# Performance work log

Measured on AMD Instinct MI355X. Metric: run time of the kernel, lower is better.

Reference implementation:

```python
import jax, jax.numpy as jnp
import numpy as np

N = 4096      # nodes
E = 131072    # edges
C_IN = 128
HID = 128     # d_model of transformer (= embed_dim used in reshape_to_trans)
OUT = 32      # GNN output channels -> transformer seq_len
HEADS = 8
DH = HID // HEADS
FF = 2048     # torch TransformerEncoderLayer default dim_feedforward
EPS = 1e-5


def layer_norm(x, g, b):
    mu = jnp.mean(x, axis=-1, keepdims=True)
    var = jnp.mean(jnp.square(x - mu), axis=-1, keepdims=True)
    return (x - mu) * jax.lax.rsqrt(var + EPS) * g + b


def setup_inputs() -> dict:
    key = jax.random.key(0)
    ks = jax.random.split(key, 24)
    def rn(k, shape, scale=0.05):
        return jax.random.normal(k, shape, dtype=jnp.float32) * scale
    inp = {
        "x": jax.random.normal(ks[0], (N, C_IN), dtype=jnp.float32),
        "edge_index": jax.random.randint(ks[1], (2, E), 0, N, dtype=jnp.int64),
        # GCN layers
        "Wg1": rn(ks[2], (C_IN, HID)), "bg1": jnp.zeros((HID,), jnp.float32),
        "Wg2": rn(ks[3], (HID, HID)),  "bg2": jnp.zeros((HID,), jnp.float32),
        "Wg3": rn(ks[4], (HID, OUT)),  "bg3": jnp.zeros((OUT,), jnp.float32),
        # MHA
        "Wq": rn(ks[5], (HID, HID)), "bq": jnp.zeros((HID,), jnp.float32),
        "Wk": rn(ks[6], (HID, HID)), "bk": jnp.zeros((HID,), jnp.float32),
        "Wv": rn(ks[7], (HID, HID)), "bv": jnp.zeros((HID,), jnp.float32),
        "Wo": rn(ks[8], (HID, HID)), "bo": jnp.zeros((HID,), jnp.float32),
        "ln1_g": jnp.ones((HID,), jnp.float32), "ln1_b": jnp.zeros((HID,), jnp.float32),
        # FFN
        "W1": rn(ks[9], (HID, FF)),  "b1": jnp.zeros((FF,), jnp.float32),
        "W2": rn(ks[10], (FF, HID)), "b2": jnp.zeros((HID,), jnp.float32),
        "ln2_g": jnp.ones((HID,), jnp.float32), "ln2_b": jnp.zeros((HID,), jnp.float32),
    }
    return inp


def reference(x, edge_index, Wg1, bg1, Wg2, bg2, Wg3, bg3,
              Wq, bq, Wk, bk, Wv, bv, Wo, bo, ln1_g, ln1_b,
              W1, b1, W2, b2, ln2_g, ln2_b):
    # ---- GCN normalization (add self-loops, symmetric D^-1/2 (A+I) D^-1/2) ----
    loop = jnp.arange(N, dtype=edge_index.dtype)
    src = jnp.concatenate([edge_index[0], loop])
    dst = jnp.concatenate([edge_index[1], loop])
    deg = jax.ops.segment_sum(jnp.ones((E + N,), jnp.float32), dst, num_segments=N)
    dinv = jnp.where(deg > 0, jax.lax.rsqrt(deg), 0.0)
    norm = (dinv[src] * dinv[dst])[:, None]  # [E+N, 1]

    def gcn(h, W, b):
        m = h @ W                               # [N, d_out]
        agg = jax.ops.segment_sum(m[src] * norm, dst, num_segments=N)
        return agg + b

    h = jax.nn.relu(gcn(x, Wg1, bg1))
    h = jax.nn.relu(gcn(h, Wg2, bg2))
    h = jax.nn.relu(gcn(h, Wg3, bg3))           # [N, OUT]

    # ---- reshape_to_trans: [N, OUT] -> [N, OUT, HID] (repeat along embed dim) ----
    t = jnp.broadcast_to(h[:, :, None], (N, OUT, HID))

    # ---- TransformerEncoderLayer (post-norm, relu FFN, no dropout at eval) ----
    q = (t @ Wq + bq).reshape(N, OUT, HEADS, DH)
    k = (t @ Wk + bk).reshape(N, OUT, HEADS, DH)
    v = (t @ Wv + bv).reshape(N, OUT, HEADS, DH)
    scores = jnp.einsum("bqhd,bkhd->bhqk", q, k) / jnp.sqrt(jnp.float32(DH))
    attn = jax.nn.softmax(scores, axis=-1)
    ctx = jnp.einsum("bhqk,bkhd->bqhd", attn, v).reshape(N, OUT, HID)
    a = ctx @ Wo + bo
    x1 = layer_norm(t + a, ln1_g, ln1_b)
    f = jax.nn.relu(x1 @ W1 + b1) @ W2 + b2
    out = layer_norm(x1 + f, ln2_g, ln2_b)      # [N, OUT, HID]
    return out
```

## Files before the change

kernel.cpp:

```cpp
#include <hip/hip_runtime.h>

#define NN 4096
#define EE 131072
#define FFD 2048

typedef float f32x4 __attribute__((ext_vector_type(4)));
typedef __bf16 bf16x8 __attribute__((ext_vector_type(8)));
typedef unsigned int u32;
typedef u32 u32x4 __attribute__((ext_vector_type(4)));
typedef unsigned short u16;
typedef u16 u16x8 __attribute__((ext_vector_type(8)));

__device__ __forceinline__ u16 f2bf(float f) {
    unsigned u = __builtin_bit_cast(unsigned, f);
    return (u16)((u + 0x7FFFu + ((u >> 16) & 1u)) >> 16);
}
__device__ __forceinline__ float bf2f(u16 h) {
    unsigned u = ((unsigned)h) << 16;
    return __builtin_bit_cast(float, u);
}

#define GLD16(g, l) __builtin_amdgcn_global_load_lds(                            \
    (const __attribute__((address_space(1))) void*)(g),                          \
    (__attribute__((address_space(3))) void*)(l), 16, 0, 0)

__global__ void k_detect(const int* __restrict__ ei, int* __restrict__ flag) {
    int v = ei[2 * threadIdx.x + 1];
    unsigned long long any = __ballot(v != 0);
    if (threadIdx.x == 0) *flag = (any == 0ULL) ? 1 : 0;
}
__device__ __forceinline__ int ldedge(const int* ei, int idx, int is64) {
    return is64 ? ei[2 * idx] : ei[idx];
}

__global__ void k_degi(const int* __restrict__ ei, const int* __restrict__ flag,
                       int* __restrict__ cnt) {
    int e = blockIdx.x * 256 + threadIdx.x;
    if (e >= EE) return;
    atomicAdd(&cnt[ldedge(ei, EE + e, *flag)], 1);
}
__global__ __launch_bounds__(1024) void k_scan(const int* __restrict__ cnt,
        int* __restrict__ rp, int* __restrict__ cur, float* __restrict__ dinv) {
    __shared__ int tsum[1024];
    int t = threadIdx.x;
    int c0 = cnt[t * 4], c1 = cnt[t * 4 + 1], c2 = cnt[t * 4 + 2], c3 = cnt[t * 4 + 3];
    int s = c0 + c1 + c2 + c3;
    tsum[t] = s;
    dinv[t * 4]     = rsqrtf((float)c0 + 1.0f);
    dinv[t * 4 + 1] = rsqrtf((float)c1 + 1.0f);
    dinv[t * 4 + 2] = rsqrtf((float)c2 + 1.0f);
    dinv[t * 4 + 3] = rsqrtf((float)c3 + 1.0f);
    __syncthreads();
    for (int off = 1; off < 1024; off <<= 1) {
        int v = (t >= off) ? tsum[t - off] : 0;
        __syncthreads();
        tsum[t] += v;
        __syncthreads();
    }
    int excl = tsum[t] - s;
    int p0 = excl, p1 = excl + c0, p2 = p1 + c1, p3 = p2 + c2;
    rp[t * 4] = p0; rp[t * 4 + 1] = p1; rp[t * 4 + 2] = p2; rp[t * 4 + 3] = p3;
    cur[t * 4] = p0; cur[t * 4 + 1] = p1; cur[t * 4 + 2] = p2; cur[t * 4 + 3] = p3;
    if (t == 1023) rp[4096] = excl + s;
}
__global__ void k_bucket(const int* __restrict__ ei, const int* __restrict__ flag,
                         int* __restrict__ cur, int* __restrict__ es) {
    int e = blockIdx.x * 256 + threadIdx.x;
    if (e >= EE) return;
    int is64 = *flag;
    int s = ldedge(ei, e, is64), d = ldedge(ei, EE + e, is64);
    int pos = atomicAdd(&cur[d], 1);
    es[pos] = s;
}

__global__ __launch_bounds__(256) void k_gcn_mm128(const float* __restrict__ h,
        const float* __restrict__ W, const float* __restrict__ dinv, float* __restrict__ ms) {
    __shared__ float hr[2][128];
    int t = threadIdx.x, n0 = blockIdx.x * 2, r = t >> 7, e = t & 127;
    hr[r][e] = h[(size_t)(n0 + r) * 128 + e];
    __syncthreads();
    float a = 0.f;
    #pragma unroll 8
    for (int c = 0; c < 128; ++c) a += hr[r][c] * W[c * 128 + e];
    ms[(size_t)(n0 + r) * 128 + e] = a * dinv[n0 + r];
}
__global__ __launch_bounds__(256) void k_gcn_mm32(const float* __restrict__ h,
        const float* __restrict__ W, const float* __restrict__ dinv, float* __restrict__ ms) {
    __shared__ float hr[8][128];
    int t = threadIdx.x, n0 = blockIdx.x * 8;
    for (int k2 = 0; k2 < 4; ++k2) {
        int idx = k2 * 256 + t;
        hr[idx >> 7][idx & 127] = h[(size_t)n0 * 128 + idx];
    }
    __syncthreads();
    int r = t >> 5, e = t & 31;
    float a = 0.f;
    #pragma unroll 8
    for (int c = 0; c < 128; ++c) a += hr[r][c] * W[c * 32 + e];
    ms[(size_t)(n0 + r) * 32 + e] = a * dinv[n0 + r];
}

__global__ __launch_bounds__(256) void k_gath128(const int* __restrict__ es,
        const int* __restrict__ rp, const float* __restrict__ ms,
        const float* __restrict__ dinv, const float* __restrict__ b,
        float* __restrict__ hout) {
    int node = blockIdx.x * 4 + (threadIdx.x >> 6), lane = threadIdx.x & 63;
    int st = rp[node], en = rp[node + 1];
    const float2* m2 = (const float2*)ms;
    float ax0 = 0.f, ay0 = 0.f, ax1 = 0.f, ay1 = 0.f;
    int e = st;
    for (; e + 2 <= en; e += 2) {
        int s0 = es[e], s1 = es[e + 1];
        float2 v0 = m2[(size_t)s0 * 64 + lane];
        float2 v1 = m2[(size_t)s1 * 64 + lane];
        ax0 += v0.x; ay0 += v0.y; ax1 += v1.x; ay1 += v1.y;
    }
    if (e < en) {
        float2 v = m2[(size_t)es[e] * 64 + lane];
        ax0 += v.x; ay0 += v.y;
    }
    float dv = dinv[node];
    float2 self = m2[(size_t)node * 64 + lane];
    int c = lane * 2;
    hout[(size_t)node * 128 + c]     = fmaxf(dv * (ax0 + ax1 + self.x) + b[c], 0.f);
    hout[(size_t)node * 128 + c + 1] = fmaxf(dv * (ay0 + ay1 + self.y) + b[c + 1], 0.f);
}
__global__ __launch_bounds__(256) void k_gath32(const int* __restrict__ es,
        const int* __restrict__ rp, const float* __restrict__ ms,
        const float* __restrict__ dinv, const float* __restrict__ b,
        float* __restrict__ hout) {
    int node = blockIdx.x * 8 + (threadIdx.x >> 5), sl = threadIdx.x & 31;
    int st = rp[node], en = rp[node + 1];
    float a0 = 0.f, a1 = 0.f;
    int e = st;
    for (; e + 2 <= en; e += 2) {
        a0 += ms[(size_t)es[e] * 32 + sl];
        a1 += ms[(size_t)es[e + 1] * 32 + sl];
    }
    if (e < en) a0 += ms[(size_t)es[e] * 32 + sl];
    float dv = dinv[node];
    hout[(size_t)node * 32 + sl] =
        fmaxf(dv * (a0 + a1 + ms[(size_t)node * 32 + sl]) + b[sl], 0.f);
}

__global__ __launch_bounds__(128) void k_prep(const float* __restrict__ Wq, const float* __restrict__ bq,
        const float* __restrict__ Wk, const float* __restrict__ bk,
        const float* __restrict__ Wv, const float* __restrict__ bv,
        const float* __restrict__ Wo, const float* __restrict__ bo, float* __restrict__ tc) {
    __shared__ float s_q[128], s_k[128], s_v[128];
    int t = threadIdx.x;
    float aq = 0, ak = 0, av = 0;
    for (int c = 0; c < 128; ++c) {
        aq += Wq[c * 128 + t]; ak += Wk[c * 128 + t]; av += Wv[c * 128 + t];
    }
    s_q[t] = aq; s_k[t] = ak; s_v[t] = av;
    tc[t] = aq; tc[128 + t] = ak; tc[256 + t] = av;
    __syncthreads();
    float pb = 0;
    for (int d = 0; d < 128; ++d) pb += bv[d] * Wo[d * 128 + t];
    tc[1440 + t] = pb + bo[t];
    for (int hh = 0; hh < 8; ++hh) {
        float p = 0;
        #pragma unroll
        for (int d = hh * 16; d < hh * 16 + 16; ++d) p += s_v[d] * Wo[d * 128 + t];
        tc[416 + hh * 128 + t] = p;
    }
    if (t < 8) {
        float A = 0, B = 0, C = 0, D = 0;
        #pragma unroll
        for (int d = t * 16; d < t * 16 + 16; ++d) {
            A += s_q[d] * s_k[d]; B += s_q[d] * bk[d];
            C += bq[d] * s_k[d];  D += bq[d] * bk[d];
        }
        tc[384 + t] = A; tc[392 + t] = B; tc[400 + t] = C; tc[408 + t] = D;
    }
}

__global__ void k_wt(const float* __restrict__ W1, const float* __restrict__ W2,
                     u16* __restrict__ w1t, u16* __restrict__ w2t) {
    int b = blockIdx.x;
    int t = (b & 1023) * 256 + threadIdx.x;
    if (b < 1024) { int f = t >> 7, c = t & 127; w1t[t] = f2bf(W1[c * 2048 + f]); }
    else          { int o = t >> 11, f = t & 2047; w2t[t] = f2bf(W2[f * 128 + o]); }
}

__global__ __launch_bounds__(256) void k_attn(const float* __restrict__ h3, const float* __restrict__ tc,
        const float* __restrict__ g1, const float* __restrict__ b1n, u16* __restrict__ x1b) {
    __shared__ float sh[32];
    __shared__ float ws_[8][32];
    int n = blockIdx.x, t = threadIdx.x;
    if (t < 32) sh[t] = h3[(size_t)n * 32 + t];
    __syncthreads();
    {
        int hh = t >> 5, i = t & 31;
        float A = tc[384 + hh], C = tc[400 + hh];
        float coef = (sh[i] * A + C) * 0.25f;
        float m = -1e30f;
        #pragma unroll
        for (int j = 0; j < 32; ++j) m = fmaxf(m, coef * sh[j]);
        float s = 0.f, wsum = 0.f;
        #pragma unroll
        for (int j = 0; j < 32; ++j) {
            float e = __expf(coef * sh[j] - m);
            s += e; wsum += e * sh[j];
        }
        ws_[hh][i] = wsum / s;
    }
    __syncthreads();
    int wave = t >> 6, lane = t & 63;
    float pb0 = tc[1440 + lane], pb1 = tc[1440 + lane + 64];
    float po0[8], po1[8];
    #pragma unroll
    for (int hh = 0; hh < 8; ++hh) {
        po0[hh] = tc[416 + hh * 128 + lane];
        po1[hh] = tc[416 + hh * 128 + lane + 64];
    }
    float ga = g1[lane], gb = g1[lane + 64], ba = b1n[lane], bb = b1n[lane + 64];
    for (int i = wave; i < 32; i += 4) {
        float y0 = sh[i] + pb0, y1 = sh[i] + pb1;
        #pragma unroll
        for (int hh = 0; hh < 8; ++hh) {
            float w = ws_[hh][i];
            y0 += w * po0[hh]; y1 += w * po1[hh];
        }
        float s1 = y0 + y1, s2 = y0 * y0 + y1 * y1;
        #pragma unroll
        for (int off = 1; off < 64; off <<= 1) {
            s1 += __shfl_xor(s1, off); s2 += __shfl_xor(s2, off);
        }
        float mu = s1 * (1.f / 128.f);
        float var = s2 * (1.f / 128.f) - mu * mu;
        float rs = rsqrtf(var + 1e-5f);
        size_t base = ((size_t)n * 32 + i) * 128;
        x1b[base + lane]      = f2bf((y0 - mu) * rs * ga + ba);
        x1b[base + lane + 64] = f2bf((y1 - mu) * rs * gb + bb);
    }
}


#define STAGE32(buf, Fb) {                                                       \
    char* db_ = (char*)(buf);                                                    \
    _Pragma("unroll") for (int c1_ = 0; c1_ < 2; ++c1_) {                        \
        int f_ = c1_ * 16 + (t >> 4);                                            \
        int bo_ = ((t & 15) * 16) ^ ((f_ & 7) << 4);                             \
        GLD16(w1t + (size_t)((Fb) + f_) * 128 + (bo_ >> 1),                      \
              db_ + c1_ * 4096 + wave * 1024);                                   \
    }                                                                            \
    _Pragma("unroll") for (int c2_ = 0; c2_ < 2; ++c2_) {                        \
        int op_ = c2_ * 32 + wave * 8 + ((t >> 3) & 7);                          \
        int pb_ = (t & 7) ^ ((t >> 3) & 7);                                      \
        int o_  = op_ * 2 + (pb_ >> 2);                                          \
        GLD16(w2t + (size_t)o_ * 2048 + (Fb) + (pb_ & 3) * 8,                    \
              db_ + 8192 + c2_ * 4096 + wave * 1024);                            \
    } }

#define FCOMP32(buf, Fb) {                                                       \
    const char* wb_ = (const char*)(buf);                                        \
    bf16x8 w2f_[8];                                                              \
    _Pragma("unroll") for (int c2_ = 0; c2_ < 8; ++c2_)                          \
        w2f_[c2_] = *(const bf16x8*)(wb_ + 8192 + (c2_ * 8 + (li >> 1)) * 128 +  \
            ((((li & 1) * 64) + g * 16) ^ ((li >> 1) << 4)));                    \
    _Pragma("unroll") for (int cf_ = 0; cf_ < 2; ++cf_) {                        \
        bf16x8 w1f_[4];                                                          \
        _Pragma("unroll") for (int ks_ = 0; ks_ < 4; ++ks_)                      \
            w1f_[ks_] = *(const bf16x8*)(wb_ + (cf_ * 16 + li) * 256 +           \
                ((ks_ * 64 + g * 16) ^ ((li & 7) << 4)));                        \
        f32x4 a0_ = (f32x4){0.f, 0.f, 0.f, 0.f};                                 \
        f32x4 a1_ = (f32x4){0.f, 0.f, 0.f, 0.f};                                 \
        _Pragma("unroll") for (int ks_ = 0; ks_ < 4; ++ks_) {                    \
            a0_ = __builtin_amdgcn_mfma_f32_16x16x32_bf16(af[0][ks_], w1f_[ks_], a0_, 0, 0, 0); \
            a1_ = __builtin_amdgcn_mfma_f32_16x16x32_bf16(af[1][ks_], w1f_[ks_], a1_, 0, 0, 0); \
        }                                                                        \
        float bias_ = b1[(Fb) + cf_ * 16 + li];                                  \
        _Pragma("unroll") for (int r_ = 0; r_ < 4; ++r_) {                       \
            int rp_ = g * 2 + (r_ >> 1);                                         \
            int w_ = (((r_ & 1) * 64) + (cf_ * 16 + li) * 2) ^ (rp_ << 4);       \
            *(u16*)(hwb + rp_ * 128 + w_)       = f2bf(fmaxf(a0_[r_] + bias_, 0.f)); \
            *(u16*)(hwb + (8 + rp_) * 128 + w_) = f2bf(fmaxf(a1_[r_] + bias_, 0.f)); \
        }                                                                        \
    }                                                                            \
    {                                                                            \
        bf16x8 a2_[2];                                                           \
        _Pragma("unroll") for (int rf_ = 0; rf_ < 2; ++rf_)                      \
            a2_[rf_] = *(const bf16x8*)(hwb + (rf_ * 8 + (li >> 1)) * 128 +      \
                ((((li & 1) * 64) + g * 16) ^ ((li >> 1) << 4)));                \
        _Pragma("unroll") for (int c2_ = 0; c2_ < 8; ++c2_) {                    \
            acc2[0][c2_] = __builtin_amdgcn_mfma_f32_16x16x32_bf16(a2_[0], w2f_[c2_], acc2[0][c2_], 0, 0, 0); \
            acc2[1][c2_] = __builtin_amdgcn_mfma_f32_16x16x32_bf16(a2_[1], w2f_[c2_], acc2[1][c2_], 0, 0, 0); \
        }                                                                        \
    } }

__global__ __launch_bounds__(256, 3) void k_ffn(const u16* __restrict__ x1b,
        const u16* __restrict__ w1t, const u16* __restrict__ w2t,
        const float* __restrict__ b1, const float* __restrict__ b2,
        const float* __restrict__ g2, const float* __restrict__ bt2, float* __restrict__ out) {
    __shared__ u16 wA[8192];
    __shared__ u16 wB[8192];
    __shared__ u16 hid[4][1024];
    int t = threadIdx.x, wave = t >> 6, lane = t & 63;
    int g = lane >> 4, li = lane & 15;
    size_t rowbase = (size_t)blockIdx.x * 128;
    char* hwb = (char*)&hid[wave][0];

    STAGE32(wA, 0);

    bf16x8 af[2][4];
    #pragma unroll
    for (int rf = 0; rf < 2; ++rf)
    #pragma unroll
    for (int ks = 0; ks < 4; ++ks)
        af[rf][ks] = *(const bf16x8*)(x1b +
            (rowbase + wave * 32 + rf * 16 + li) * 128 + ks * 32 + g * 8);

    f32x4 acc2[2][8];
    #pragma unroll
    for (int a = 0; a < 2; ++a)
    #pragma unroll
    for (int b = 0; b < 8; ++b) acc2[a][b] = (f32x4){0.f, 0.f, 0.f, 0.f};

    __syncthreads();

    for (int F = 0; F < FFD; F += 64) {
        STAGE32(wB, F + 32);
        FCOMP32(wA, F);
        __syncthreads();
        if (F + 64 < FFD) STAGE32(wA, F + 64);
        FCOMP32(wB, F + 32);
        __syncthreads();
    }

    #pragma unroll
    for (int rf = 0; rf < 2; ++rf)
    #pragma unroll
    for (int r = 0; r < 4; ++r) {
        int lrow = wave * 32 + rf * 16 + g * 4 + r;
        size_t grow = rowbase + lrow;
        float vals[8], s1 = 0.f, s2 = 0.f;
        #pragma unroll
        for (int cf2 = 0; cf2 < 8; ++cf2) {
            int col = cf2 * 16 + li;
            float xv = bf2f(x1b[grow * 128 + col]);
            float y = xv + acc2[rf][cf2][r] + b2[col];
            vals[cf2] = y; s1 += y; s2 += y * y;
        }
        #pragma unroll
        for (int m = 1; m < 16; m <<= 1) {
            s1 += __shfl_xor(s1, m); s2 += __shfl_xor(s2, m);
        }
        float mu = s1 * (1.f / 128.f);
        float var = s2 * (1.f / 128.f) - mu * mu;
        float rs = rsqrtf(var + 1e-5f);
        #pragma unroll
        for (int cf2 = 0; cf2 < 8; ++cf2) {
            int col = cf2 * 16 + li;
            out[grow * 128 + col] = (vals[cf2] - mu) * rs * g2[col] + bt2[col];
        }
    }
}

extern "C" void kernel_launch(void* const* d_in, const int* in_sizes, int n_in,
                              void* d_out, int out_size, void* d_ws, size_t ws_size,
                              hipStream_t stream) {
    const float* x   = (const float*)d_in[0];
    const int*   ei  = (const int*)d_in[1];
    const float *Wg1 = (const float*)d_in[2],  *bg1 = (const float*)d_in[3];
    const float *Wg2 = (const float*)d_in[4],  *bg2 = (const float*)d_in[5];
    const float *Wg3 = (const float*)d_in[6],  *bg3 = (const float*)d_in[7];
    const float *Wq  = (const float*)d_in[8],  *bq  = (const float*)d_in[9];
    const float *Wk  = (const float*)d_in[10], *bk  = (const float*)d_in[11];
    const float *Wv  = (const float*)d_in[12], *bv  = (const float*)d_in[13];
    const float *Wo  = (const float*)d_in[14], *bo  = (const float*)d_in[15];
    const float *g1  = (const float*)d_in[16], *b1n = (const float*)d_in[17];
    const float *W1  = (const float*)d_in[18], *b1  = (const float*)d_in[19];
    const float *W2  = (const float*)d_in[20], *b2  = (const float*)d_in[21];
    const float *g2  = (const float*)d_in[22], *bt2 = (const float*)d_in[23];

    char* ws = (char*)d_ws;
    int*   flag = (int*)(ws + 0);
    int*   cnt  = (int*)(ws + 4096);
    int*   rp   = (int*)(ws + 20480);
    int*   cur  = (int*)(ws + 40960);
    float* dinv = (float*)(ws + 57344);
    float* ms   = (float*)(ws + 73728);
    int*   es   = (int*)(ws + 2170880);
    float* hA   = (float*)(ws + 2695168);
    float* hB   = (float*)(ws + 4792320);
    float* tc   = (float*)(ws + 6889472);
    u16*   w1t  = (u16*)(ws + 6897664);
    u16*   w2t  = (u16*)(ws + 7421952);
    u16*   x1b  = (u16*)(ws + 8388608);
    float* out  = (float*)d_out;

    k_detect<<<1, 64, 0, stream>>>(ei, flag);
    hipMemsetAsync(cnt, 0, 16384, stream);
    k_degi<<<512, 256, 0, stream>>>(ei, flag, cnt);
    k_scan<<<1, 1024, 0, stream>>>(cnt, rp, cur, dinv);
    k_bucket<<<512, 256, 0, stream>>>(ei, flag, cur, es);

    k_gcn_mm128<<<2048, 256, 0, stream>>>(x, Wg1, dinv, ms);
    k_gath128<<<1024, 256, 0, stream>>>(es, rp, ms, dinv, bg1, hA);
    k_gcn_mm128<<<2048, 256, 0, stream>>>(hA, Wg2, dinv, ms);
    k_gath128<<<1024, 256, 0, stream>>>(es, rp, ms, dinv, bg2, hB);
    k_gcn_mm32<<<512, 256, 0, stream>>>(hB, Wg3, dinv, ms);
    k_gath32<<<512, 256, 0, stream>>>(es, rp, ms, dinv, bg3, hA);

    k_prep<<<1, 128, 0, stream>>>(Wq, bq, Wk, bk, Wv, bv, Wo, bo, tc);
    k_wt<<<2048, 256, 0, stream>>>(W1, W2, w1t, w2t);

    k_attn<<<4096, 256, 0, stream>>>(hA, tc, g1, b1n, x1b);

    k_ffn<<<1024, 256, 0, stream>>>(x1b, w1t, w2t, b1, b2, g2, bt2, out);
}
```

Baseline: 307.1 us.

## Fuse independent setup kernels into one launch and pack bf16 conversions in FFN

Merges flag detection with the count zeroing, replacing the memset, and combines edge bucketing, the first GCN matmul, the FFN weight transpose and the attention constant prep into one block-partitioned kernel. The goal is to cut launch count and the idle gaps between small serial kernels, since these jobs do not depend on each other. The FFN epilogue now uses v_cvt_pk_bf16_f32 to convert two floats per instruction instead of manual rounding. The fused kernel's shared buffer and barriers are sized for the largest branch, and the prep branch runs as a single block that could become a tail.

```diff
diff --git a/kernel.cpp b/kernel.cpp
--- a/kernel.cpp
+++ b/kernel.cpp
@@ -19,18 +19,31 @@
     unsigned u = ((unsigned)h) << 16;
     return __builtin_bit_cast(float, u);
 }
+__device__ __forceinline__ u32 cvtpk(float lo, float hi) {
+    u32 r;
+    asm("v_cvt_pk_bf16_f32 %0, %1, %2" : "=v"(r) : "v"(lo), "v"(hi));
+    return r;
+}
 
 #define GLD16(g, l) __builtin_amdgcn_global_load_lds(                            \
     (const __attribute__((address_space(1))) void*)(g),                          \
     (__attribute__((address_space(3))) void*)(l), 16, 0, 0)
 
-__global__ void k_detect(const int* __restrict__ ei, int* __restrict__ flag) {
-    int v = ei[2 * threadIdx.x + 1];
-    unsigned long long any = __ballot(v != 0);
-    if (threadIdx.x == 0) *flag = (any == 0ULL) ? 1 : 0;
-}
 __device__ __forceinline__ int ldedge(const int* ei, int idx, int is64) {
     return is64 ? ei[2 * idx] : ei[idx];
+}
+
+__global__ void k_init(const int* __restrict__ ei, int* __restrict__ flag,
+                       int* __restrict__ cnt) {
+    if (blockIdx.x == 0) {
+        if (threadIdx.x < 64) {
+            int v = ei[2 * threadIdx.x + 1];
+            unsigned long long any = __ballot(v != 0);
+            if (threadIdx.x == 0) *flag = (any == 0ULL) ? 1 : 0;
+        }
+    } else {
+        cnt[(blockIdx.x - 1) * 256 + threadIdx.x] = 0;
+    }
 }
 
 __global__ void k_degi(const int* __restrict__ ei, const int* __restrict__ flag,
@@ -63,14 +76,70 @@
     cur[t * 4] = p0; cur[t * 4 + 1] = p1; cur[t * 4 + 2] = p2; cur[t * 4 + 3] = p3;
     if (t == 1023) rp[4096] = excl + s;
 }
-__global__ void k_bucket(const int* __restrict__ ei, const int* __restrict__ flag,
-                         int* __restrict__ cur, int* __restrict__ es) {
-    int e = blockIdx.x * 256 + threadIdx.x;
-    if (e >= EE) return;
-    int is64 = *flag;
-    int s = ldedge(ei, e, is64), d = ldedge(ei, EE + e, is64);
-    int pos = atomicAdd(&cur[d], 1);
-    es[pos] = s;
+
+__global__ __launch_bounds__(256) void k_fuse1(const int* __restrict__ ei,
+        const int* __restrict__ flag, int* __restrict__ cur, int* __restrict__ es,
+        const float* __restrict__ x, const float* __restrict__ Wg1,
+        const float* __restrict__ dinv, float* __restrict__ ms,
+        const float* __restrict__ W1, const float* __restrict__ W2,
+        u16* __restrict__ w1t, u16* __restrict__ w2t,
+        const float* __restrict__ Wq, const float* __restrict__ bq,
+        const float* __restrict__ Wk, const float* __restrict__ bk,
+        const float* __restrict__ Wv, const float* __restrict__ bv,
+        const float* __restrict__ Wo, const float* __restrict__ bo,
+        float* __restrict__ tc) {
+    __shared__ float sm[384];
+    int b = blockIdx.x, t = threadIdx.x;
+    if (b < 512) {
+        int e = b * 256 + t;
+        int is64 = *flag;
+        int s = ldedge(ei, e, is64), d = ldedge(ei, EE + e, is64);
+        int pos = atomicAdd(&cur[d], 1);
+        es[pos] = s;
+    } else if (b < 2560) {
+        int n0 = (b - 512) * 2, r = t >> 7, e = t & 127;
+        sm[r * 128 + e] = x[(size_t)(n0 + r) * 128 + e];
+        __syncthreads();
+        float a = 0.f;
+        #pragma unroll 8
+        for (int c = 0; c < 128; ++c) a += sm[r * 128 + c] * Wg1[c * 128 + e];
+        ms[(size_t)(n0 + r) * 128 + e] = a * dinv[n0 + r];
+    } else if (b < 4608) {
+        int bb = b - 2560;
+        int tg = (bb & 1023) * 256 + t;
+        if (bb < 1024) { int f = tg >> 7, c = tg & 127; w1t[tg] = f2bf(W1[c * 2048 + f]); }
+        else           { int o = tg >> 11, f = tg & 2047; w2t[tg] = f2bf(W2[f * 128 + o]); }
+    } else {
+        float aq = 0, ak = 0, av = 0;
+        if (t < 128) {
+            for (int c = 0; c < 128; ++c) {
+                aq += Wq[c * 128 + t]; ak += Wk[c * 128 + t]; av += Wv[c * 128 + t];
+            }
+            sm[t] = aq; sm[128 + t] = ak; sm[256 + t] = av;
+            tc[t] = aq; tc[128 + t] = ak; tc[256 + t] = av;
+        }
+        __syncthreads();
+        if (t < 128) {
+            float pb = 0;
+            for (int d = 0; d < 128; ++d) pb += bv[d] * Wo[d * 128 + t];
+            tc[1440 + t] = pb + bo[t];
+            for (int hh = 0; hh < 8; ++hh) {
+                float p = 0;
+                #pragma unroll
+                for (int d = hh * 16; d < hh * 16 + 16; ++d) p += sm[256 + d] * Wo[d * 128 + t];
+                tc[416 + hh * 128 + t] = p;
+            }
+        }
+        if (t < 8) {
+            float A = 0, B = 0, C = 0, D = 0;
+            #pragma unroll
+            for (int d = t * 16; d < t * 16 + 16; ++d) {
+                A += sm[d] * sm[128 + d]; B += sm[d] * bk[d];
+                C += bq[d] * sm[128 + d]; D += bq[d] * bk[d];
+            }
+            tc[384 + t] = A; tc[392 + t] = B; tc[400 + t] = C; tc[408 + t] = D;
+        }
+    }
 }
 
 __global__ __launch_bounds__(256) void k_gcn_mm128(const float* __restrict__ h,
@@ -141,47 +210,6 @@
     float dv = dinv[node];
     hout[(size_t)node * 32 + sl] =
         fmaxf(dv * (a0 + a1 + ms[(size_t)node * 32 + sl]) + b[sl], 0.f);
-}
-
-__global__ __launch_bounds__(128) void k_prep(const float* __restrict__ Wq, const float* __restrict__ bq,
-        const float* __restrict__ Wk, const float* __restrict__ bk,
-        const float* __restrict__ Wv, const float* __restrict__ bv,
-        const float* __restrict__ Wo, const float* __restrict__ bo, float* __restrict__ tc) {
-    __shared__ float s_q[128], s_k[128], s_v[128];
-    int t = threadIdx.x;
-    float aq = 0, ak = 0, av = 0;
-    for (int c = 0; c < 128; ++c) {
-        aq += Wq[c * 128 + t]; ak += Wk[c * 128 + t]; av += Wv[c * 128 + t];
-    }
-    s_q[t] = aq; s_k[t] = ak; s_v[t] = av;
-    tc[t] = aq; tc[128 + t] = ak; tc[256 + t] = av;
-    __syncthreads();
-    float pb = 0;
-    for (int d = 0; d < 128; ++d) pb += bv[d] * Wo[d * 128 + t];
-    tc[1440 + t] = pb + bo[t];
-    for (int hh = 0; hh < 8; ++hh) {
-        float p = 0;
-        #pragma unroll
-        for (int d = hh * 16; d < hh * 16 + 16; ++d) p += s_v[d] * Wo[d * 128 + t];
-        tc[416 + hh * 128 + t] = p;
-    }
-    if (t < 8) {
-        float A = 0, B = 0, C = 0, D = 0;
-        #pragma unroll
-        for (int d = t * 16; d < t * 16 + 16; ++d) {
-            A += s_q[d] * s_k[d]; B += s_q[d] * bk[d];
-            C += bq[d] * s_k[d];  D += bq[d] * bk[d];
-        }
-        tc[384 + t] = A; tc[392 + t] = B; tc[400 + t] = C; tc[408 + t] = D;
-    }
-}
-
-__global__ void k_wt(const float* __restrict__ W1, const float* __restrict__ W2,
-                     u16* __restrict__ w1t, u16* __restrict__ w2t) {
-    int b = blockIdx.x;
-    int t = (b & 1023) * 256 + threadIdx.x;
-    if (b < 1024) { int f = t >> 7, c = t & 127; w1t[t] = f2bf(W1[c * 2048 + f]); }
-    else          { int o = t >> 11, f = t & 2047; w2t[t] = f2bf(W2[f * 128 + o]); }
 }
 
 __global__ __launch_bounds__(256) void k_attn(const float* __restrict__ h3, const float* __restrict__ tc,
@@ -271,13 +299,22 @@
             a0_ = __builtin_amdgcn_mfma_f32_16x16x32_bf16(af[0][ks_], w1f_[ks_], a0_, 0, 0, 0); \
             a1_ = __builtin_amdgcn_mfma_f32_16x16x32_bf16(af[1][ks_], w1f_[ks_], a1_, 0, 0, 0); \
         }                                                                        \
-        float bias_ = b1[(Fb) + cf_ * 16 + li];                                  \
-        _Pragma("unroll") for (int r_ = 0; r_ < 4; ++r_) {                       \
-            int rp_ = g * 2 + (r_ >> 1);                                         \
-            int w_ = (((r_ & 1) * 64) + (cf_ * 16 + li) * 2) ^ (rp_ << 4);       \
-            *(u16*)(hwb + rp_ * 128 + w_)       = f2bf(fmaxf(a0_[r_] + bias_, 0.f)); \
-            *(u16*)(hwb + (8 + rp_) * 128 + w_) = f2bf(fmaxf(a1_[r_] + bias_, 0.f)); \
-        }                                                                        \
+        float4 bb_;                                                              \
+        bb_.x = b1[(Fb) + cf_ * 16 + li];                                        \
+        u32 pkA0 = cvtpk(fmaxf(a0_[0] + bb_.x, 0.f), fmaxf(a0_[1] + bb_.x, 0.f)); \
+        u32 pkA1 = cvtpk(fmaxf(a0_[2] + bb_.x, 0.f), fmaxf(a0_[3] + bb_.x, 0.f)); \
+        u32 pkB0 = cvtpk(fmaxf(a1_[0] + bb_.x, 0.f), fmaxf(a1_[1] + bb_.x, 0.f)); \
+        u32 pkB1 = cvtpk(fmaxf(a1_[2] + bb_.x, 0.f), fmaxf(a1_[3] + bb_.x, 0.f)); \
+        int rp0_ = g * 2, rp1_ = g * 2 + 1;                                      \
+        int wl_ = (cf_ * 16 + li) * 2;                                           \
+        *(u16*)(hwb + rp0_ * 128 + ((wl_) ^ (rp0_ << 4)))        = (u16)pkA0;    \
+        *(u16*)(hwb + rp0_ * 128 + ((64 + wl_) ^ (rp0_ << 4)))   = (u16)(pkA0 >> 16); \
+        *(u16*)(hwb + rp1_ * 128 + ((wl_) ^ (rp1_ << 4)))        = (u16)pkA1;    \
+        *(u16*)(hwb + rp1_ * 128 + ((64 + wl_) ^ (rp1_ << 4)))   = (u16)(pkA1 >> 16); \
+        *(u16*)(hwb + (8 + rp0_) * 128 + ((wl_) ^ (rp0_ << 4)))      = (u16)pkB0; \
+        *(u16*)(hwb + (8 + rp0_) * 128 + ((64 + wl_) ^ (rp0_ << 4))) = (u16)(pkB0 >> 16); \
+        *(u16*)(hwb + (8 + rp1_) * 128 + ((wl_) ^ (rp1_ << 4)))      = (u16)pkB1; \
+        *(u16*)(hwb + (8 + rp1_) * 128 + ((64 + wl_) ^ (rp1_ << 4))) = (u16)(pkB1 >> 16); \
     }                                                                            \
     {                                                                            \
         bf16x8 a2_[2];                                                           \
@@ -391,22 +428,20 @@
     u16*   x1b  = (u16*)(ws + 8388608);
     float* out  = (float*)d_out;
 
-    k_detect<<<1, 64, 0, stream>>>(ei, flag);
-    hipMemsetAsync(cnt, 0, 16384, stream);
+    k_init<<<17, 256, 0, stream>>>(ei, flag, cnt);
     k_degi<<<512, 256, 0, stream>>>(ei, flag, cnt);
     k_scan<<<1, 1024, 0, stream>>>(cnt, rp, cur, dinv);
-    k_bucket<<<512, 256, 0, stream>>>(ei, flag, cur, es);
-
-    k_gcn_mm128<<<2048, 256, 0, stream>>>(x, Wg1, dinv, ms);
+
+    k_fuse1<<<4609, 256, 0, stream>>>(ei, flag, cur, es, x, Wg1, dinv, ms,
+                                      W1, W2, w1t, w2t,
+                                      Wq, bq, Wk, bk, Wv, bv, Wo, bo, tc);
+
     k_gath128<<<1024, 256, 0, stream>>>(es, rp, ms, dinv, bg1, hA);
     k_gcn_mm128<<<2048, 256, 0, stream>>>(hA, Wg2, dinv, ms);
     k_gath128<<<1024, 256, 0, stream>>>(es, rp, ms, dinv, bg2, hB);
     k_gcn_mm32<<<512, 256, 0, stream>>>(hB, Wg3, dinv, ms);
     k_gath32<<<512, 256, 0, stream>>>(es, rp, ms, dinv, bg3, hA);
 
-    k_prep<<<1, 128, 0, stream>>>(Wq, bq, Wk, bk, Wv, bv, Wo, bo, tc);
-    k_wt<<<2048, 256, 0, stream>>>(W1, W2, w1t, w2t);
-
     k_attn<<<4096, 256, 0, stream>>>(hA, tc, g1, b1n, x1b);
 
     k_ffn<<<1024, 256, 0, stream>>>(x1b, w1t, w2t, b1, b2, g2, bt2, out);
```

Result: faster. 288.0 us (-6.2%).
